# Kernel optimization log

Hardware: AMD Instinct MI355X
Metric: run time of the kernel (lower is better)

The kernel has to match this reference:

```python
import jax, jax.numpy as jnp
import numpy as np

B, S, HID = 2, 2048, 2048
NH, HD, RD = 16, 128, 64
KVC, QC = 512, 1536


def _apply_rope(t):
    # t: [B, H, S, R]; standard half-split rotary embedding
    R = t.shape[-1]
    s = t.shape[-2]
    inv_freq = 1.0 / (10000.0 ** (jnp.arange(0, R, 2, dtype=jnp.float32) / R))  # [R/2]
    ang = jnp.arange(s, dtype=jnp.float32)[:, None] * inv_freq[None, :]  # [S, R/2]
    cos, sin = jnp.cos(ang), jnp.sin(ang)
    t1, t2 = t[..., : R // 2], t[..., R // 2 :]
    return jnp.concatenate([t1 * cos - t2 * sin, t2 * cos + t1 * sin], axis=-1)


def setup_inputs() -> dict:
    key = jax.random.key(0)
    ks = jax.random.split(key, 20)

    def lin(k, fan_in, fan_out):
        bound = 1.0 / np.sqrt(fan_in)
        kw, kb = jax.random.split(k)
        W = jax.random.uniform(kw, (fan_in, fan_out), jnp.float32, -bound, bound)
        b = jax.random.uniform(kb, (fan_out,), jnp.float32, -bound, bound)
        return W, b

    x = jax.random.normal(ks[0], (B, S, HID), jnp.float32)
    W_kvd, b_kvd = lin(ks[1], HID, KVC)
    W_ku, b_ku = lin(ks[2], KVC, NH * HD)
    W_vu, b_vu = lin(ks[3], KVC, NH * HD)
    W_kr, b_kr = lin(ks[4], KVC, NH * RD)
    W_qd, b_qd = lin(ks[5], HID, QC)
    W_qu, b_qu = lin(ks[6], QC, NH * HD)
    W_qr, b_qr = lin(ks[7], QC, NH * RD)
    W_o, b_o = lin(ks[8], NH * HD, HID)
    return dict(x=x, W_kvd=W_kvd, b_kvd=b_kvd, W_ku=W_ku, b_ku=b_ku,
                W_vu=W_vu, b_vu=b_vu, W_kr=W_kr, b_kr=b_kr,
                W_qd=W_qd, b_qd=b_qd, W_qu=W_qu, b_qu=b_qu,
                W_qr=W_qr, b_qr=b_qr, W_o=W_o, b_o=b_o)


def reference(x, W_kvd, b_kvd, W_ku, b_ku, W_vu, b_vu, W_kr, b_kr,
              W_qd, b_qd, W_qu, b_qu, W_qr, b_qr, W_o, b_o):
    b, s, _ = x.shape

    def heads(t, d):  # [B,S,NH*d] -> [B,NH,S,d]
        return t.reshape(b, s, NH, d).transpose(0, 2, 1, 3)

    kv_c = x @ W_kvd + b_kvd                     # [B,S,KVC]
    keys_c = heads(kv_c @ W_ku + b_ku, HD)       # [B,H,S,HD]
    values = heads(kv_c @ W_vu + b_vu, HD)
    keys_r = _apply_rope(heads(kv_c @ W_kr + b_kr, RD))

    q_c = x @ W_qd + b_qd                        # [B,S,QC]
    queries_c = heads(q_c @ W_qu + b_qu, HD)
    queries_r = _apply_rope(heads(q_c @ W_qr + b_qr, RD))

    q = jnp.concatenate([queries_c, queries_r], axis=-1)  # [B,H,S,HD+RD]
    k = jnp.concatenate([keys_c, keys_r], axis=-1)

    scale = 1.0 / np.sqrt(HD + RD)
    scores = jnp.einsum('bhqd,bhkd->bhqk', q, k) * scale
    causal = jnp.triu(jnp.ones((s, s), dtype=bool), k=1)
    scores = jnp.where(causal[None, None], jnp.float32(-1e9), scores)
    probs = jax.nn.softmax(scores, axis=-1)
    ctx = jnp.einsum('bhqk,bhkd->bhqd', probs, values)    # [B,H,S,HD]
    ctx = ctx.transpose(0, 2, 1, 3).reshape(b, s, NH * HD)
    return ctx @ W_o + b_o
```

## Files before the change

### kernel.cpp

```cpp
#include <hip/hip_runtime.h>
#include <math.h>

#define BB   2
#define SS   2048
#define HIDD 2048
#define NHH  16
#define HDD  128
#define RDD  64
#define KVCC 512
#define QCC  1536
#define DQK  192
#define MROWS 4096

using bf16x8 = __attribute__((ext_vector_type(8))) short;
using short4v = __attribute__((ext_vector_type(4))) short;
using f32x4  = __attribute__((ext_vector_type(4))) float;
using f32x16 = __attribute__((ext_vector_type(16))) float;

static __device__ __forceinline__ float b2f(short s) {
    unsigned u = ((unsigned)(unsigned short)s) << 16;
    union { unsigned u; float f; } v; v.u = u; return v.f;
}
static __device__ __forceinline__ short f2b(float f) {
    union { float f; unsigned u; } v; v.f = f;
    unsigned r = (v.u + 0x7fffu + ((v.u >> 16) & 1u)) >> 16;
    return (short)r;
}
static __device__ __forceinline__ unsigned cvtpk(float lo, float hi) {
    unsigned r;
    asm("v_cvt_pk_bf16_f32 %0, %1, %2" : "=v"(r) : "v"(lo), "v"(hi));
    return r;
}

#define GLOAD16(gsrc, ldst) \
    __builtin_amdgcn_global_load_lds((const __attribute__((address_space(1))) void*)(gsrc), \
                                     (__attribute__((address_space(3))) void*)(ldst), 16, 0, 0)

__global__ void cvt_kernel(const float* __restrict__ in, short* __restrict__ out) {
    int i = (blockIdx.x * blockDim.x + threadIdx.x) * 4;
    float4 v = *(const float4*)(in + i);
    short4v o;
    o[0] = f2b(v.x); o[1] = f2b(v.y); o[2] = f2b(v.z); o[3] = f2b(v.w);
    *(short4v*)(out + i) = o;
}

__global__ void wtrans_kernel(
    const float* __restrict__ W0, const float* __restrict__ W1,
    const float* __restrict__ W2, const float* __restrict__ W3,
    const float* __restrict__ W4, const float* __restrict__ W5,
    const float* __restrict__ W6, const float* __restrict__ W7,
    short* __restrict__ D0, short* __restrict__ D1,
    short* __restrict__ D2, short* __restrict__ D3) {
    __shared__ float t[32][33];
    int bid = blockIdx.x;
    const float* W; short* Dst; int K, N, lt;
    if (bid < 4096) {
        if (bid < 1024) { W = W0; Dst = D0;                        K = 2048; N = 512;  lt = bid; }
        else            { W = W1; Dst = D0 + (size_t)512 * 2048;   K = 2048; N = 1536; lt = bid - 1024; }
    } else if (bid < 6656) {
        if (bid < 5120)      { W = W2; Dst = D1;                       K = 512; N = 2048; lt = bid - 4096; }
        else if (bid < 6144) { W = W3; Dst = D1 + (size_t)2048 * 512;  K = 512; N = 2048; lt = bid - 5120; }
        else                 { W = W4; Dst = D1 + (size_t)4096 * 512;  K = 512; N = 1024; lt = bid - 6144; }
    } else if (bid < 11264) {
        if (bid < 9728) { W = W5; Dst = D2;                        K = 1536; N = 2048; lt = bid - 6656; }
        else            { W = W6; Dst = D2 + (size_t)2048 * 1536;  K = 1536; N = 1024; lt = bid - 9728; }
    } else { W = W7; Dst = D3; K = 2048; N = 2048; lt = bid - 11264; }
    int ntx = N >> 5;
    int n0 = (lt % ntx) * 32, k0 = (lt / ntx) * 32;
    int tx = threadIdx.x, ty = threadIdx.y;
#pragma unroll
    for (int i = 0; i < 4; i++)
        t[ty + i * 8][tx] = W[(size_t)(k0 + ty + i * 8) * N + n0 + tx];
    __syncthreads();
#pragma unroll
    for (int i = 0; i < 4; i++)
        Dst[(size_t)(n0 + ty + i * 8) * K + k0 + tx] = f2b(t[tx][ty + i * 8]);
}

template <int ID>
__global__ __launch_bounds__(256) void gemm128(
    const short* __restrict__ A, const short* __restrict__ Bt,
    const float* __restrict__ b0, const float* __restrict__ b1, const float* __restrict__ b2,
    void* __restrict__ C0, void* __restrict__ C1,
    int M, int N, int K) {
    __shared__ short Asm[4096];
    __shared__ short Bsm[4096];
    int tid = threadIdx.x, lane = tid & 63, w = tid >> 6;
    int wm = w >> 1, wn = w & 1;
    int m0 = blockIdx.y * 128, n0 = blockIdx.x * 128;
    int fr = lane & 15, fk = (lane >> 4) * 8;
    const short* Ag = A + (size_t)(m0 + (tid >> 2)) * K + (tid & 3) * 8;
    const short* Bg = Bt + (size_t)(n0 + (tid >> 2)) * K + (tid & 3) * 8;
    f32x4 acc[4][4] = {};
    for (int k0 = 0; k0 < K; k0 += 32) {
        __syncthreads();
        GLOAD16(Ag + k0, &Asm[tid * 8]);
        GLOAD16(Ag + k0 + (size_t)64 * K, &Asm[2048 + tid * 8]);
        GLOAD16(Bg + k0, &Bsm[tid * 8]);
        GLOAD16(Bg + k0 + (size_t)64 * K, &Bsm[2048 + tid * 8]);
        __syncthreads();
        bf16x8 af[4], bfv[4];
#pragma unroll
        for (int m = 0; m < 4; m++)
            af[m] = *(const bf16x8*)&Asm[(wm * 64 + m * 16 + fr) * 32 + fk];
#pragma unroll
        for (int n = 0; n < 4; n++)
            bfv[n] = *(const bf16x8*)&Bsm[(wn * 64 + n * 16 + fr) * 32 + fk];
#pragma unroll
        for (int m = 0; m < 4; m++)
#pragma unroll
            for (int n = 0; n < 4; n++)
                acc[m][n] = __builtin_amdgcn_mfma_f32_16x16x32_bf16(af[m], bfv[n], acc[m][n], 0, 0, 0);
    }
#pragma unroll
    for (int m = 0; m < 4; m++)
#pragma unroll
        for (int n = 0; n < 4; n++)
#pragma unroll
            for (int r = 0; r < 4; r++) {
                int row = m0 + wm * 64 + m * 16 + ((lane >> 4) << 2) + r;
                int col = n0 + wn * 64 + n * 16 + fr;
                float v = acc[m][n][r];
                if constexpr (ID == 0) {
                    ((float*)C0)[(size_t)row * N + col] = v + b0[col];
                } else if constexpr (ID == 1) {
                    if (col < KVCC)
                        ((short*)C0)[(size_t)row * KVCC + col] = f2b(v + b0[col]);
                    else
                        ((short*)C1)[(size_t)row * QCC + (col - KVCC)] = f2b(v + b1[col - KVCC]);
                } else if constexpr (ID == 2) {
                    int b = row >> 11, s = row & (SS - 1);
                    if (col < 2048) {
                        int h = col >> 7, d = col & 127;
                        ((short*)C0)[(((size_t)(b * NHH + h)) * SS + s) * DQK + d] = f2b(v + b0[col]);
                    } else if (col < 4096) {
                        int c = col - 2048; int h = c >> 7, d = c & 127;
                        ((short*)C1)[(((size_t)(b * NHH + h)) * HDD + d) * SS + s] = f2b(v + b1[c]);
                    } else {
                        int c = col - 4096; int h = c >> 6, d = c & 63;
                        ((short*)C0)[(((size_t)(b * NHH + h)) * SS + s) * DQK + HDD + d] = f2b(v + b2[c]);
                    }
                } else {
                    int b = row >> 11, s = row & (SS - 1);
                    if (col < 2048) {
                        int h = col >> 7, d = col & 127;
                        ((short*)C0)[(((size_t)(b * NHH + h)) * SS + s) * DQK + d] = f2b(v + b0[col]);
                    } else {
                        int c = col - 2048; int h = c >> 6, d = c & 63;
                        ((short*)C0)[(((size_t)(b * NHH + h)) * SS + s) * DQK + HDD + d] = f2b(v + b1[c]);
                    }
                }
            }
}

__global__ void rope_kernel(short* __restrict__ Tk, short* __restrict__ Tq) {
    int idx = blockIdx.x * blockDim.x + threadIdx.x;
    const int HALF = BB * NHH * SS * 32;
    short* T = (idx < HALF) ? Tk : Tq;
    int id = (idx < HALF) ? idx : idx - HALF;
    int i = id & 31;
    int s = (id >> 5) & (SS - 1);
    int bh = id >> 16;
    short* p = T + ((size_t)bh * SS + s) * DQK + HDD;
    float t1 = b2f(p[i]), t2 = b2f(p[i + 32]);
    float inv = exp2f(-(float)i * 0.41524101186092034f);
    float ang = (float)s * inv;
    float sn, cs;
    sincosf(ang, &sn, &cs);
    p[i] = f2b(t1 * cs - t2 * sn);
    p[i + 32] = f2b(t2 * cs + t1 * sn);
}

__global__ __launch_bounds__(256, 2) void attn_kernel(
    const short* __restrict__ Q, const short* __restrict__ Kg,
    const short* __restrict__ Vt, short* __restrict__ ctx) {
    __shared__ short Ksm[2][64 * 192];
    __shared__ short Vsm[2][128 * 64];
    int tid = threadIdx.x, lane = tid & 63, w = tid >> 6;
    int hf = lane >> 5, l31 = lane & 31;
    int bid = blockIdx.x;
    int half = bid >> 8, a = (bid & 255) >> 5;
    int qt = half ? a : 15 - a;
    int bh = bid & 31;
    int bb = bh >> 4, hd = bh & 15;
    int q0 = qt * 128;
    const short* Qp = Q + (size_t)bh * SS * DQK;
    const short* Kp = Kg + (size_t)bh * SS * DQK;
    const char*  Vp = (const char*)(Vt + (size_t)bh * HDD * SS);
    int wr0 = q0 + w * 32;
    int qrow = wr0 + l31;
    const float scale = 0.07216878364870323f;
    const float L2E = 1.44269504088896f;

    bf16x8 qf[12];
#pragma unroll
    for (int s = 0; s < 12; s++)
        qf[s] = *(const bf16x8*)(Qp + (size_t)qrow * DQK + s * 16 + hf * 8);

    f32x16 acc[4] = {};
    float mrow = -1e30f, lsum = 0.f;
    int nt = 2 * qt + 2;

    auto stageK = [&](int key0, int b) {
#pragma unroll
        for (int pp = 0; pp < 6; pp++) {
            int flat = pp * 4096 + tid * 16;
            int row = flat / 384, bir = flat - row * 384;
            const char* src = (const char*)Kp + (size_t)(key0 + row) * 384 + (bir ^ ((row & 7) << 4));
            GLOAD16(src, (char*)Ksm[b] + flat);
        }
    };
    auto stageV = [&](int key0, int b) {
#pragma unroll
        for (int c = 0; c < 4; c++) {
            int flat = c * 4096 + tid * 16;
            int d = flat >> 7, bik = flat & 127;
            const char* src = Vp + (size_t)d * (SS * 2) + (size_t)key0 * 2 + (bik ^ ((d & 7) << 4));
            GLOAD16(src, (char*)Vsm[b] + flat);
        }
    };

    stageK(0, 0); stageV(0, 0);
    __syncthreads();

    for (int t0 = 0; t0 < nt; t0++) {
        int key0 = t0 * 64;
        int cur = t0 & 1;
        if (t0 + 1 < nt) { stageK(key0 + 64, cur ^ 1); stageV(key0 + 64, cur ^ 1); }
        bool active = (key0 <= wr0 + 31);
        if (active) {
            f32x16 z = {};
            f32x16 sv0 = z, sv1 = z;
            int xr = (l31 & 7) << 4;
            const char* Kb = (const char*)Ksm[cur];
            __builtin_amdgcn_s_setprio(1);
#pragma unroll
            for (int s = 0; s < 12; s++) {
                bf16x8 k0 = *(const bf16x8*)(Kb + l31 * 384 + ((s * 32 + hf * 16) ^ xr));
                bf16x8 k1 = *(const bf16x8*)(Kb + (32 + l31) * 384 + ((s * 32 + hf * 16) ^ xr));
                sv0 = __builtin_amdgcn_mfma_f32_32x32x16_bf16(k0, qf[s], sv0, 0, 0, 0);
                sv1 = __builtin_amdgcn_mfma_f32_32x32x16_bf16(k1, qf[s], sv1, 0, 0, 0);
            }
            __builtin_amdgcn_s_setprio(0);
            bool domask = (key0 + 63 > wr0);
            float p[32];
            float pmax = -1e30f;
#pragma unroll
            for (int t = 0; t < 2; t++)
#pragma unroll
                for (int r = 0; r < 16; r++) {
                    float v = (t ? sv1[r] : sv0[r]) * scale;
                    int key = key0 + 32 * t + (r & 3) + 8 * (r >> 2) + 4 * hf;
                    if (domask && key > qrow) v = -1e30f;
                    p[t * 16 + r] = v;
                    pmax = fmaxf(pmax, v);
                }
            if (__any(pmax > mrow + 8.f)) {
                float pc = fmaxf(pmax, __shfl_xor(pmax, 32, 64));
                float mn = fmaxf(mrow, pc);
                float al = exp2f((mrow - mn) * L2E);
                mrow = mn;
                lsum *= al;
                float arl[16];
#pragma unroll
                for (int r = 0; r < 16; r++)
                    arl[r] = __shfl(al, (r & 3) + 8 * (r >> 2) + 4 * hf, 64);
#pragma unroll
                for (int n = 0; n < 4; n++)
#pragma unroll
                    for (int r = 0; r < 16; r++)
                        acc[n][r] *= arl[r];
            }
#pragma unroll
            for (int i = 0; i < 32; i++) {
                p[i] = exp2f((p[i] - mrow) * L2E);
                lsum += p[i];
            }
            const char* Vb = (const char*)Vsm[cur];
#pragma unroll
            for (int g = 0; g < 4; g++) {
                int base = (g >> 1) * 16 + (g & 1) * 8;
                unsigned a01 = cvtpk(p[base + 0], p[base + 1]);
                unsigned a23 = cvtpk(p[base + 2], p[base + 3]);
                unsigned b01 = cvtpk(p[base + 4], p[base + 5]);
                unsigned b23 = cvtpk(p[base + 6], p[base + 7]);
                unsigned s0 = hf ? a01 : b01, s1 = hf ? a23 : b23;
                unsigned r0 = (unsigned)__shfl_xor((int)s0, 32, 64);
                unsigned r1 = (unsigned)__shfl_xor((int)s1, 32, 64);
                union { unsigned u[4]; bf16x8 v; } af;
                af.u[0] = hf ? r0 : a01;
                af.u[1] = hf ? r1 : a23;
                af.u[2] = hf ? b01 : r0;
                af.u[3] = hf ? b23 : r1;
                __builtin_amdgcn_s_setprio(1);
#pragma unroll
                for (int n = 0; n < 4; n++) {
                    int d = n * 32 + l31;
                    bf16x8 vf = *(const bf16x8*)(Vb + d * 128 + ((g * 32 + hf * 16) ^ ((d & 7) << 4)));
                    acc[n] = __builtin_amdgcn_mfma_f32_32x32x16_bf16(af.v, vf, acc[n], 0, 0, 0);
                }
                __builtin_amdgcn_s_setprio(0);
            }
        }
        __syncthreads();
    }
    lsum += __shfl_xor(lsum, 32, 64);
    float rc = 1.0f / lsum;
    float rcl[16];
#pragma unroll
    for (int r = 0; r < 16; r++)
        rcl[r] = __shfl(rc, (r & 3) + 8 * (r >> 2) + 4 * hf, 64);
#pragma unroll
    for (int n = 0; n < 4; n++)
#pragma unroll
        for (int r = 0; r < 16; r++) {
            int row = wr0 + (r & 3) + 8 * (r >> 2) + 4 * hf;
            int d = n * 32 + l31;
            ctx[((size_t)(bb * SS + row)) * (NHH * HDD) + hd * HDD + d] = f2b(acc[n][r] * rcl[r]);
        }
}

extern "C" void kernel_launch(void* const* d_in, const int* in_sizes, int n_in,
                              void* d_out, int out_size, void* d_ws, size_t ws_size,
                              hipStream_t stream) {
    const float* x     = (const float*)d_in[0];
    const float* W_kvd = (const float*)d_in[1];  const float* b_kvd = (const float*)d_in[2];
    const float* W_ku  = (const float*)d_in[3];  const float* b_ku  = (const float*)d_in[4];
    const float* W_vu  = (const float*)d_in[5];  const float* b_vu  = (const float*)d_in[6];
    const float* W_kr  = (const float*)d_in[7];  const float* b_kr  = (const float*)d_in[8];
    const float* W_qd  = (const float*)d_in[9];  const float* b_qd  = (const float*)d_in[10];
    const float* W_qu  = (const float*)d_in[11]; const float* b_qu  = (const float*)d_in[12];
    const float* W_qr  = (const float*)d_in[13]; const float* b_qr  = (const float*)d_in[14];
    const float* W_o   = (const float*)d_in[15]; const float* b_o   = (const float*)d_in[16];
    float* out = (float*)d_out;

    char* p = (char*)d_ws;
    auto alloc = [&](size_t elems) {
        short* r = (short*)p;
        p += ((elems * 2) + 255) & ~(size_t)255;
        return r;
    };
    short* xb   = alloc((size_t)MROWS * HIDD);
    short* kvc  = alloc((size_t)MROWS * KVCC);
    short* qc   = alloc((size_t)MROWS * QCC);
    short* kbuf = alloc((size_t)BB * NHH * SS * DQK);
    short* qbuf = alloc((size_t)BB * NHH * SS * DQK);
    short* vtb  = alloc((size_t)BB * NHH * HDD * SS);
    short* ctx  = alloc((size_t)MROWS * NHH * HDD);
    short* Wt1  = alloc((size_t)2048 * 2048);
    short* Wt2  = alloc((size_t)5120 * 512);
    short* Wt3  = alloc((size_t)3072 * 1536);
    short* Wt4  = alloc((size_t)2048 * 2048);

    cvt_kernel<<<dim3((MROWS * HIDD) / 1024), dim3(256), 0, stream>>>(x, xb);
    dim3 tb(32, 8);
    wtrans_kernel<<<dim3(15360), tb, 0, stream>>>(
        W_kvd, W_qd, W_ku, W_vu, W_kr, W_qu, W_qr, W_o, Wt1, Wt2, Wt3, Wt4);

    gemm128<1><<<dim3(2048 / 128, MROWS / 128), 256, 0, stream>>>(
        xb, Wt1, b_kvd, b_qd, nullptr, kvc, qc, MROWS, 2048, 2048);
    gemm128<2><<<dim3(5120 / 128, MROWS / 128), 256, 0, stream>>>(
        kvc, Wt2, b_ku, b_vu, b_kr, kbuf, vtb, MROWS, 5120, 512);
    gemm128<3><<<dim3(3072 / 128, MROWS / 128), 256, 0, stream>>>(
        qc, Wt3, b_qu, b_qr, nullptr, qbuf, nullptr, MROWS, 3072, 1536);

    rope_kernel<<<dim3((2 * BB * NHH * SS * 32) / 256), dim3(256), 0, stream>>>(kbuf, qbuf);

    attn_kernel<<<dim3(512), 256, 0, stream>>>(qbuf, kbuf, vtb, ctx);

    gemm128<0><<<dim3(HIDD / 128, MROWS / 128), 256, 0, stream>>>(
        ctx, Wt4, b_o, nullptr, nullptr, out, nullptr, MROWS, HIDD, NHH * HDD);
}
```

Measured before the change: 417.2 us.

## Deepen GEMM K-tile, transpose V separately, and restructure attention softmax loops

The GEMM K-step grows from 32 to 64, which halves the number of barrier pairs per tile and doubles LDS use per block. The V projection now writes row-major, and a separate tiled transpose kernel produces the V^T layout, replacing the strided scattered stores in the GEMM epilogue. In attention, the softmax scale is folded into a single fma before exp2, max and sum use tree reductions, and all P fragments are built before one batched run of PV MFMAs. The extra kernel adds a launch and a full V round trip through memory, and the larger LDS footprint may lower GEMM occupancy.

Result: slower. 434.4 us (+4.1%).

```diff
diff --git a/kernel.cpp b/kernel.cpp
--- a/kernel.cpp
+++ b/kernel.cpp
@@ -77,40 +77,60 @@
         Dst[(size_t)(n0 + ty + i * 8) * K + k0 + tx] = f2b(t[tx][ty + i * 8]);
 }
 
+__global__ void vtrans_kernel(const short* __restrict__ in, short* __restrict__ outp) {
+    __shared__ short t[32][33];
+    int bh = blockIdx.z;
+    int s0 = blockIdx.x * 32, d0 = blockIdx.y * 32;
+    int tx = threadIdx.x, ty = threadIdx.y;
+    const short* ip = in + (size_t)bh * SS * HDD;
+    short* op = outp + (size_t)bh * HDD * SS;
+#pragma unroll
+    for (int i = 0; i < 4; i++)
+        t[ty + i * 8][tx] = ip[(size_t)(s0 + ty + i * 8) * HDD + d0 + tx];
+    __syncthreads();
+#pragma unroll
+    for (int i = 0; i < 4; i++)
+        op[(size_t)(d0 + ty + i * 8) * SS + s0 + tx] = t[tx][ty + i * 8];
+}
+
 template <int ID>
 __global__ __launch_bounds__(256) void gemm128(
     const short* __restrict__ A, const short* __restrict__ Bt,
     const float* __restrict__ b0, const float* __restrict__ b1, const float* __restrict__ b2,
     void* __restrict__ C0, void* __restrict__ C1,
     int M, int N, int K) {
-    __shared__ short Asm[4096];
-    __shared__ short Bsm[4096];
+    __shared__ short Asm[8192];
+    __shared__ short Bsm[8192];
     int tid = threadIdx.x, lane = tid & 63, w = tid >> 6;
     int wm = w >> 1, wn = w & 1;
     int m0 = blockIdx.y * 128, n0 = blockIdx.x * 128;
     int fr = lane & 15, fk = (lane >> 4) * 8;
-    const short* Ag = A + (size_t)(m0 + (tid >> 2)) * K + (tid & 3) * 8;
-    const short* Bg = Bt + (size_t)(n0 + (tid >> 2)) * K + (tid & 3) * 8;
     f32x4 acc[4][4] = {};
-    for (int k0 = 0; k0 < K; k0 += 32) {
+    for (int k0 = 0; k0 < K; k0 += 64) {
         __syncthreads();
-        GLOAD16(Ag + k0, &Asm[tid * 8]);
-        GLOAD16(Ag + k0 + (size_t)64 * K, &Asm[2048 + tid * 8]);
-        GLOAD16(Bg + k0, &Bsm[tid * 8]);
-        GLOAD16(Bg + k0 + (size_t)64 * K, &Bsm[2048 + tid * 8]);
+#pragma unroll
+        for (int pp = 0; pp < 4; pp++) {
+            int flat = pp * 4096 + tid * 16;
+            int row = flat >> 7, cb = (flat & 127) >> 1;
+            GLOAD16(A + (size_t)(m0 + row) * K + k0 + cb, (char*)Asm + flat);
+            GLOAD16(Bt + (size_t)(n0 + row) * K + k0 + cb, (char*)Bsm + flat);
+        }
         __syncthreads();
-        bf16x8 af[4], bfv[4];
-#pragma unroll
-        for (int m = 0; m < 4; m++)
-            af[m] = *(const bf16x8*)&Asm[(wm * 64 + m * 16 + fr) * 32 + fk];
-#pragma unroll
-        for (int n = 0; n < 4; n++)
-            bfv[n] = *(const bf16x8*)&Bsm[(wn * 64 + n * 16 + fr) * 32 + fk];
-#pragma unroll
-        for (int m = 0; m < 4; m++)
+#pragma unroll
+        for (int ks = 0; ks < 2; ks++) {
+            bf16x8 af[4], bfv[4];
+#pragma unroll
+            for (int m = 0; m < 4; m++)
+                af[m] = *(const bf16x8*)&Asm[(wm * 64 + m * 16 + fr) * 64 + ks * 32 + fk];
 #pragma unroll
             for (int n = 0; n < 4; n++)
-                acc[m][n] = __builtin_amdgcn_mfma_f32_16x16x32_bf16(af[m], bfv[n], acc[m][n], 0, 0, 0);
+                bfv[n] = *(const bf16x8*)&Bsm[(wn * 64 + n * 16 + fr) * 64 + ks * 32 + fk];
+#pragma unroll
+            for (int m = 0; m < 4; m++)
+#pragma unroll
+                for (int n = 0; n < 4; n++)
+                    acc[m][n] = __builtin_amdgcn_mfma_f32_16x16x32_bf16(af[m], bfv[n], acc[m][n], 0, 0, 0);
+        }
     }
 #pragma unroll
     for (int m = 0; m < 4; m++)
@@ -135,7 +155,7 @@
                         ((short*)C0)[(((size_t)(b * NHH + h)) * SS + s) * DQK + d] = f2b(v + b0[col]);
                     } else if (col < 4096) {
                         int c = col - 2048; int h = c >> 7, d = c & 127;
-                        ((short*)C1)[(((size_t)(b * NHH + h)) * HDD + d) * SS + s] = f2b(v + b1[c]);
+                        ((short*)C1)[(((size_t)(b * NHH + h)) * SS + s) * HDD + d] = f2b(v + b1[c]);
                     } else {
                         int c = col - 4096; int h = c >> 6, d = c & 63;
                         ((short*)C0)[(((size_t)(b * NHH + h)) * SS + s) * DQK + HDD + d] = f2b(v + b2[c]);
@@ -244,19 +264,25 @@
             __builtin_amdgcn_s_setprio(0);
             bool domask = (key0 + 63 > wr0);
             float p[32];
-            float pmax = -1e30f;
 #pragma unroll
             for (int t = 0; t < 2; t++)
 #pragma unroll
                 for (int r = 0; r < 16; r++) {
-                    float v = (t ? sv1[r] : sv0[r]) * scale;
+                    float v = (t ? sv1[r] : sv0[r]);
                     int key = key0 + 32 * t + (r & 3) + 8 * (r >> 2) + 4 * hf;
                     if (domask && key > qrow) v = -1e30f;
                     p[t * 16 + r] = v;
-                    pmax = fmaxf(pmax, v);
                 }
-            if (__any(pmax > mrow + 8.f)) {
-                float pc = fmaxf(pmax, __shfl_xor(pmax, 32, 64));
+            float tm[16];
+#pragma unroll
+            for (int i = 0; i < 16; i++) tm[i] = fmaxf(p[i], p[i + 16]);
+#pragma unroll
+            for (int i = 0; i < 8; i++) tm[i] = fmaxf(tm[i], tm[i + 8]);
+#pragma unroll
+            for (int i = 0; i < 4; i++) tm[i] = fmaxf(tm[i], tm[i + 4]);
+            float pmaxs = fmaxf(fmaxf(tm[0], tm[1]), fmaxf(tm[2], tm[3])) * scale;
+            if (__any(pmaxs > mrow + 8.f)) {
+                float pc = fmaxf(pmaxs, __shfl_xor(pmaxs, 32, 64));
                 float mn = fmaxf(mrow, pc);
                 float al = exp2f((mrow - mn) * L2E);
                 mrow = mn;
@@ -271,12 +297,19 @@
                     for (int r = 0; r < 16; r++)
                         acc[n][r] *= arl[r];
             }
-#pragma unroll
-            for (int i = 0; i < 32; i++) {
-                p[i] = exp2f((p[i] - mrow) * L2E);
-                lsum += p[i];
-            }
-            const char* Vb = (const char*)Vsm[cur];
+            float sL = scale * L2E, mL = mrow * L2E;
+#pragma unroll
+            for (int i = 0; i < 32; i++)
+                p[i] = exp2f(fmaf(p[i], sL, -mL));
+            float ts[16];
+#pragma unroll
+            for (int i = 0; i < 16; i++) ts[i] = p[i] + p[i + 16];
+#pragma unroll
+            for (int i = 0; i < 8; i++) ts[i] = ts[i] + ts[i + 8];
+#pragma unroll
+            for (int i = 0; i < 4; i++) ts[i] = ts[i] + ts[i + 4];
+            lsum += (ts[0] + ts[1]) + (ts[2] + ts[3]);
+            bf16x8 afv[4];
 #pragma unroll
             for (int g = 0; g < 4; g++) {
                 int base = (g >> 1) * 16 + (g & 1) * 8;
@@ -292,15 +325,19 @@
                 af.u[1] = hf ? r1 : a23;
                 af.u[2] = hf ? b01 : r0;
                 af.u[3] = hf ? b23 : r1;
-                __builtin_amdgcn_s_setprio(1);
+                afv[g] = af.v;
+            }
+            const char* Vb = (const char*)Vsm[cur];
+            __builtin_amdgcn_s_setprio(1);
+#pragma unroll
+            for (int g = 0; g < 4; g++)
 #pragma unroll
                 for (int n = 0; n < 4; n++) {
                     int d = n * 32 + l31;
                     bf16x8 vf = *(const bf16x8*)(Vb + d * 128 + ((g * 32 + hf * 16) ^ ((d & 7) << 4)));
-                    acc[n] = __builtin_amdgcn_mfma_f32_32x32x16_bf16(af.v, vf, acc[n], 0, 0, 0);
+                    acc[n] = __builtin_amdgcn_mfma_f32_32x32x16_bf16(afv[g], vf, acc[n], 0, 0, 0);
                 }
-                __builtin_amdgcn_s_setprio(0);
-            }
+            __builtin_amdgcn_s_setprio(0);
         }
         __syncthreads();
     }
@@ -345,6 +382,7 @@
     short* qc   = alloc((size_t)MROWS * QCC);
     short* kbuf = alloc((size_t)BB * NHH * SS * DQK);
     short* qbuf = alloc((size_t)BB * NHH * SS * DQK);
+    short* vbuf = alloc((size_t)BB * NHH * SS * HDD);
     short* vtb  = alloc((size_t)BB * NHH * HDD * SS);
     short* ctx  = alloc((size_t)MROWS * NHH * HDD);
     short* Wt1  = alloc((size_t)2048 * 2048);
@@ -360,10 +398,12 @@
     gemm128<1><<<dim3(2048 / 128, MROWS / 128), 256, 0, stream>>>(
         xb, Wt1, b_kvd, b_qd, nullptr, kvc, qc, MROWS, 2048, 2048);
     gemm128<2><<<dim3(5120 / 128, MROWS / 128), 256, 0, stream>>>(
-        kvc, Wt2, b_ku, b_vu, b_kr, kbuf, vtb, MROWS, 5120, 512);
+        kvc, Wt2, b_ku, b_vu, b_kr, kbuf, vbuf, MROWS, 5120, 512);
     gemm128<3><<<dim3(3072 / 128, MROWS / 128), 256, 0, stream>>>(
         qc, Wt3, b_qu, b_qr, nullptr, qbuf, nullptr, MROWS, 3072, 1536);
 
+    vtrans_kernel<<<dim3(SS / 32, HDD / 32, BB * NHH), tb, 0, stream>>>(vbuf, vtb);
+
     rope_kernel<<<dim3((2 * BB * NHH * SS * 32) / 256), dim3(256), 0, stream>>>(kbuf, qbuf);
 
     attn_kernel<<<dim3(512), 256, 0, stream>>>(qbuf, kbuf, vtb, ctx);
```
